# Kernel tuning notes

Measured on AMD Instinct MI355X. Metric: run time of the kernel, lower is better.

The kernel has to match this reference:

```python
import jax, jax.numpy as jnp
import numpy as np

N_NODES = 50000
N_EDGES = 640000
IN_CH = 128
HIDDEN = 128
HEADS = 4
HEAD_DIM = HIDDEN // HEADS  # 32
NEG_SLOPE = 0.2


def setup_inputs() -> dict:
    key = jax.random.key(0)
    ks = jax.random.split(key, 12)
    x = jax.random.normal(ks[0], (N_NODES, IN_CH), dtype=jnp.float32)
    edge_index = jax.random.randint(ks[1], (2, N_EDGES), 0, N_NODES, dtype=jnp.int64)
    s = 0.1
    W1 = jax.random.normal(ks[2], (IN_CH, HEADS * HEAD_DIM), dtype=jnp.float32) * s
    a_src1 = jax.random.normal(ks[3], (HEADS, HEAD_DIM), dtype=jnp.float32) * s
    a_dst1 = jax.random.normal(ks[4], (HEADS, HEAD_DIM), dtype=jnp.float32) * s
    b1 = jax.random.normal(ks[5], (HEADS * HEAD_DIM,), dtype=jnp.float32) * s
    W2 = jax.random.normal(ks[6], (HIDDEN, HEADS * HEAD_DIM), dtype=jnp.float32) * s
    a_src2 = jax.random.normal(ks[7], (HEADS, HEAD_DIM), dtype=jnp.float32) * s
    a_dst2 = jax.random.normal(ks[8], (HEADS, HEAD_DIM), dtype=jnp.float32) * s
    b2 = jax.random.normal(ks[9], (HEADS * HEAD_DIM,), dtype=jnp.float32) * s
    return {"x": x, "edge_index": edge_index, "W1": W1, "a_src1": a_src1,
            "a_dst1": a_dst1, "b1": b1, "W2": W2, "a_src2": a_src2,
            "a_dst2": a_dst2, "b2": b2}


def _gat_conv(x, src, dst, W, a_src, a_dst, b):
    """PyG GATConv (concat=True, add_self_loops already applied to src/dst)."""
    N = x.shape[0]
    H, C = a_src.shape
    h = (x @ W).reshape(N, H, C)                      # [N, H, C]
    alpha_s = jnp.einsum('nhc,hc->nh', h, a_src)      # [N, H]
    alpha_d = jnp.einsum('nhc,hc->nh', h, a_dst)      # [N, H]
    e = alpha_s[src] + alpha_d[dst]                   # [E, H]
    e = jnp.where(e > 0, e, NEG_SLOPE * e)            # leaky_relu(0.2)
    # segment softmax over destination nodes (every node has a self-loop)
    emax = jax.ops.segment_max(e, dst, num_segments=N)
    ee = jnp.exp(e - emax[dst])
    denom = jax.ops.segment_sum(ee, dst, num_segments=N)
    alpha = ee / (denom[dst] + 1e-16)                 # [E, H]
    out = jax.ops.segment_sum(h[src] * alpha[:, :, None], dst, num_segments=N)
    return out.reshape(N, H * C) + b


def reference(x, edge_index, W1, a_src1, a_dst1, b1, W2, a_src2, a_dst2, b2):
    N = x.shape[0]
    loops = jnp.arange(N, dtype=edge_index.dtype)
    src = jnp.concatenate([edge_index[0], loops])
    dst = jnp.concatenate([edge_index[1], loops])
    h = _gat_conv(x, src, dst, W1, a_src1, a_dst1, b1)
    h = jax.nn.relu(h)  # dropout is identity in eval mode
    out = _gat_conv(h, src, dst, W2, a_src2, a_dst2, b2)
    return out
```

## Files before the change

### kernel.cpp

```cpp
#include <hip/hip_runtime.h>
#include <hip/hip_bf16.h>
#include <hip/hip_fp16.h>

#define N_NODES 50000
#define N_EDGES 640000
#define E_TOT   690000
#define CH      128
#define GEMMB   782
#define EBLK    2048
#define NEB     337
#define NBUCK   196
#define MTP     344

typedef __attribute__((ext_vector_type(8))) short short8;
typedef __attribute__((ext_vector_type(4))) float float4v;

static __device__ __forceinline__ float bf2f(unsigned short u) {
  return __uint_as_float(((unsigned)u) << 16);
}
static __device__ __forceinline__ unsigned short f2bf(float f) {
  unsigned u = __float_as_uint(f);
  return (unsigned short)((u + 0x7fffu + ((u >> 16) & 1u)) >> 16);
}

__global__ void k_detect(const unsigned short* __restrict__ x16,
                         const unsigned int* __restrict__ eiw,
                         int* __restrict__ flags)
{
  __shared__ int sf32, si64;
  int t = threadIdx.x;
  if (t == 0) { sf32 = 0; si64 = 1; }
  __syncthreads();
  int bad = 0;
  for (int i = t; i < 4096; i += 256) {
    float v = bf2f(x16[i]);
    if (!(v == v) || fabsf(v) > 100.f) bad = 1;
  }
  if (bad) atomicOr(&sf32, 1);
  if (t < 128 && eiw[2 * t + 1] != 0u) atomicAnd(&si64, 0);
  __syncthreads();
  if (t == 0) { flags[0] = sf32; flags[1] = si64; }
}

static __device__ __forceinline__ void load_edge(const int* __restrict__ ei,
                                                 int e, int i64, int& s, int& d)
{
  if (e >= N_EDGES) { s = d = e - N_EDGES; return; }
  if (i64) { s = ei[2 * (size_t)e]; d = ei[2 * ((size_t)N_EDGES + e)]; }
  else     { s = ei[e];             d = ei[N_EDGES + e]; }
}

static __device__ __forceinline__ short8 load_bf8(const void* __restrict__ X,
                                                  size_t off, int f32)
{
  if (!f32) return *(const short8*)((const unsigned short*)X + off);
  const float4* p = (const float4*)((const float*)X + off);
  float4 u = p[0], v = p[1];
  short8 r;
  r[0] = (short)f2bf(u.x); r[1] = (short)f2bf(u.y);
  r[2] = (short)f2bf(u.z); r[3] = (short)f2bf(u.w);
  r[4] = (short)f2bf(v.x); r[5] = (short)f2bf(v.y);
  r[6] = (short)f2bf(v.z); r[7] = (short)f2bf(v.w);
  return r;
}

__global__ __launch_bounds__(256) void k_prep(
    const void* __restrict__ W1, const void* __restrict__ W2,
    const void* __restrict__ as1, const void* __restrict__ ad1,
    const void* __restrict__ as2, const void* __restrict__ ad2,
    unsigned short* __restrict__ Wt1, unsigned short* __restrict__ Wt2,
    unsigned short* __restrict__ Ba1, unsigned short* __restrict__ Ba2,
    const int* __restrict__ flags)
{
  int f32 = flags[0];
  int b = blockIdx.x, t = threadIdx.x;
  if (b < 8) {
    int g = b * 256 + t;
    int l = g >> 10;
    int rem = g & 1023;
    int k = rem >> 3, n = rem & 7;
    const void* W  = l ? W2 : W1;
    const void* av = (n < 4) ? (l ? as2 : as1) : (l ? ad2 : ad1);
    int h = n & 3;
    float sum = 0.f;
    for (int c = 0; c < 32; c++) {
      float w = f32 ? ((const float*)W)[k * 128 + h * 32 + c]
                    : bf2f(((const unsigned short*)W)[k * 128 + h * 32 + c]);
      float a = f32 ? ((const float*)av)[h * 32 + c]
                    : bf2f(((const unsigned short*)av)[h * 32 + c]);
      sum += w * a;
    }
    unsigned short* Ba = l ? Ba2 : Ba1;
    Ba[n * 128 + k] = f2bf(sum);
    Ba[(8 + (rem >> 7)) * 128 + (rem & 127)] = 0;
  } else {
    int b2 = b - 8;
    int l = b2 >> 7, c = b2 & 127;
    if (t < 128) {
      const void* W = l ? W2 : W1;
      unsigned short* Wt = l ? Wt2 : Wt1;
      Wt[c * 128 + t] = f32 ? f2bf(((const float*)W)[t * 128 + c])
                            : ((const unsigned short*)W)[t * 128 + c];
    }
  }
}

struct SmemG { unsigned short WB[144][136]; };

static __device__ __forceinline__ void gemm_body(
    SmemG& sm, int bx,
    const void* __restrict__ X,
    const unsigned short* __restrict__ Wt_g,
    const unsigned short* __restrict__ Ba_g,
    unsigned short* __restrict__ H, float* __restrict__ AS,
    float* __restrict__ AD, int nrows, int xf32)
{
  int tid = threadIdx.x;
#pragma unroll
  for (int i = 0; i < 8; i++) {
    int j = i * 256 + tid;
    int c = j >> 4, k8 = j & 15;
    short8 v = *(const short8*)(Wt_g + c * 128 + k8 * 8);
    *(short8*)&sm.WB[c][k8 * 8] = v;
  }
  {
    int n = tid >> 4, k8 = tid & 15;
    short8 v = *(const short8*)(Ba_g + n * 128 + k8 * 8);
    *(short8*)&sm.WB[128 + n][k8 * 8] = v;
  }
  __syncthreads();
  int wave = tid >> 6, lane = tid & 63;
  int rt = bx * 4 + wave;
  if (rt * 16 >= nrows) return;
  int R0 = rt * 16;
  int m = lane & 15, quad = lane >> 4;
  size_t abase = (size_t)(R0 + m) * CH + quad * 8;
  float4v acc[8];
  float4v accA = (float4v){0.f, 0.f, 0.f, 0.f};
#pragma unroll
  for (int t = 0; t < 8; t++) acc[t] = (float4v){0.f, 0.f, 0.f, 0.f};
#pragma unroll
  for (int kb = 0; kb < 4; kb++) {
    short8 a = load_bf8(X, abase + kb * 32, xf32);
#pragma unroll
    for (int ct = 0; ct < 8; ct++) {
      short8 b = *(const short8*)&sm.WB[ct * 16 + m][kb * 32 + quad * 8];
      acc[ct] = __builtin_amdgcn_mfma_f32_16x16x32_bf16(a, b, acc[ct], 0, 0, 0);
    }
    short8 bA = *(const short8*)&sm.WB[128 + m][kb * 32 + quad * 8];
    accA = __builtin_amdgcn_mfma_f32_16x16x32_bf16(a, bA, accA, 0, 0, 0);
  }
  int rbase = R0 + quad * 4;
#pragma unroll
  for (int ct = 0; ct < 8; ct++) {
    int col = ct * 16 + m;
#pragma unroll
    for (int r = 0; r < 4; r++)
      H[(size_t)(rbase + r) * CH + col] = __half_as_ushort(__float2half(acc[ct][r]));
  }
  if (m < 4) {
#pragma unroll
    for (int r = 0; r < 4; r++)
      AS[(size_t)(rbase + r) * 4 + m] = accA[r];
  } else if (m < 8) {
#pragma unroll
    for (int r = 0; r < 4; r++)
      AD[(size_t)(rbase + r) * 4 + (m - 4)] = accA[r];
  }
}

__global__ __launch_bounds__(256, 2) void k_gemm(
    const void* __restrict__ X,
    const unsigned short* __restrict__ Wt_g,
    const unsigned short* __restrict__ Ba_g,
    unsigned short* __restrict__ H, float* __restrict__ AS, float* __restrict__ AD,
    int nrows)
{
  __shared__ SmemG sm;
  gemm_body(sm, blockIdx.x, X, Wt_g, Ba_g, H, AS, AD, nrows, 0);
}

__global__ __launch_bounds__(256, 2) void k_gemm_hist(
    const void* __restrict__ X,
    const unsigned short* __restrict__ Wt_g,
    const unsigned short* __restrict__ Ba_g,
    unsigned short* __restrict__ H, float* __restrict__ AS, float* __restrict__ AD,
    int nrows, const int* __restrict__ ei, int* __restrict__ MT,
    const int* __restrict__ flags)
{
  __shared__ SmemG sm;
  __shared__ int hist[NBUCK];
  if (blockIdx.x >= GEMMB) {
    int b = blockIdx.x - GEMMB;
    int t = threadIdx.x;
    if (t < NBUCK) hist[t] = 0;
    __syncthreads();
    int i64 = flags[1];
    int base = b * EBLK;
#pragma unroll
    for (int k = 0; k < 8; k++) {
      int e = base + k * 256 + t;
      if (e < E_TOT) {
        int s, d;
        load_edge(ei, e, i64, s, d);
        atomicAdd(&hist[d >> 8], 1);
      }
    }
    __syncthreads();
    if (t < NBUCK) MT[t * MTP + b] = hist[t];
    return;
  }
  gemm_body(sm, blockIdx.x, X, Wt_g, Ba_g, H, AS, AD, nrows, flags[0]);
}

__global__ __launch_bounds__(512) void k_rowscan(int* __restrict__ MT,
                                                 int* __restrict__ T)
{
  __shared__ int sh[512];
  int q = blockIdx.x, t = threadIdx.x;
  int v = (t < NEB) ? MT[q * MTP + t] : 0;
  sh[t] = v;
  __syncthreads();
  for (int off = 1; off < 512; off <<= 1) {
    int u = (t >= off) ? sh[t - off] : 0;
    __syncthreads();
    sh[t] += u;
    __syncthreads();
  }
  if (t < NEB) MT[q * MTP + t] = sh[t] - v;
  if (t == NEB - 1) T[q] = sh[t];
}

__global__ __launch_bounds__(256) void k_bscan(const int* __restrict__ T,
                                               int* __restrict__ BB)
{
  __shared__ int sh[256];
  int t = threadIdx.x;
  int v = (t < NBUCK) ? T[t] : 0;
  sh[t] = v;
  __syncthreads();
  for (int off = 1; off < 256; off <<= 1) {
    int u = (t >= off) ? sh[t - off] : 0;
    __syncthreads();
    sh[t] += u;
    __syncthreads();
  }
  if (t < NBUCK) BB[t] = sh[t] - v;
  if (t == NBUCK - 1) BB[NBUCK] = sh[t];
}

__global__ __launch_bounds__(256) void k_bucket(
    const int* __restrict__ ei, const int* __restrict__ MT,
    const int* __restrict__ BB, int2* __restrict__ ebuf,
    const int* __restrict__ flags)
{
  __shared__ int cur[NBUCK];
  int b = blockIdx.x, t = threadIdx.x;
  if (t < NBUCK) cur[t] = BB[t] + MT[t * MTP + b];
  __syncthreads();
  int i64 = flags[1];
  int base = b * EBLK;
#pragma unroll
  for (int k = 0; k < 8; k++) {
    int e = base + k * 256 + t;
    if (e < E_TOT) {
      int s, d;
      load_edge(ei, e, i64, s, d);
      int pos = atomicAdd(&cur[d >> 8], 1);
      ebuf[pos] = make_int2(s, d);
    }
  }
}

__global__ __launch_bounds__(256) void k_fine(
    const int2* __restrict__ ebuf, const int* __restrict__ BB,
    int* __restrict__ row_ptr, int* __restrict__ deg,
    int* __restrict__ csr_src)
{
  __shared__ int cnt[256], sh[256], cur[256];
  int q = blockIdx.x, t = threadIdx.x;
  int lo = BB[q], hi = BB[q + 1];
  cnt[t] = 0;
  __syncthreads();
  for (int i = lo + t; i < hi; i += 256)
    atomicAdd(&cnt[ebuf[i].y & 255], 1);
  __syncthreads();
  int v = cnt[t];
  sh[t] = v;
  __syncthreads();
  for (int off = 1; off < 256; off <<= 1) {
    int u = (t >= off) ? sh[t - off] : 0;
    __syncthreads();
    sh[t] += u;
    __syncthreads();
  }
  int lp = sh[t] - v;
  int n = (q << 8) + t;
  if (n < N_NODES) { row_ptr[n] = lo + lp; deg[n] = v; }
  cur[t] = lo + lp;
  __syncthreads();
  for (int i = lo + t; i < hi; i += 256) {
    int2 p = ebuf[i];
    int slot = atomicAdd(&cur[p.y & 255], 1);
    csr_src[slot] = p.x;
  }
}

__global__ __launch_bounds__(256) void k_agg(
    const int* __restrict__ row_ptr, const int* __restrict__ deg,
    const int* __restrict__ csr_src,
    const __half* __restrict__ H,
    const float* __restrict__ AS, const float* __restrict__ AD,
    const void* __restrict__ b, void* __restrict__ Y,
    const int* __restrict__ flags, int layer)
{
  int tid = threadIdx.x;
  int node = blockIdx.x * 4 + (tid >> 6);
  if (node >= N_NODES) return;
  int lane = tid & 63;
  int h = lane >> 4;
  int c0 = 2 * lane;
  float adh = AD[(size_t)node * 4 + h];
  int start = row_ptr[node];
  int dg = deg[node];
  const __half2* __restrict__ H2 = (const __half2*)H;
  float accx = 0.f, accy = 0.f, den = 0.f;
  int j = 0;
  for (; j + 8 <= dg; j += 8) {
    int sI[8];
#pragma unroll
    for (int u = 0; u < 8; u++) sI[u] = csr_src[start + j + u];
    float eV[8];
#pragma unroll
    for (int u = 0; u < 8; u++) eV[u] = AS[(size_t)sI[u] * 4 + h] + adh;
    float2 vV[8];
#pragma unroll
    for (int u = 0; u < 8; u++) vV[u] = __half22float2(H2[(size_t)sI[u] * 64 + lane]);
#pragma unroll
    for (int u = 0; u < 8; u++) {
      float x = eV[u] > 0.f ? eV[u] : 0.2f * eV[u];
      float ex = __expf(x);
      accx += ex * vV[u].x;
      accy += ex * vV[u].y;
      den  += ex;
    }
  }
  for (; j + 4 <= dg; j += 4) {
    int sI[4];
#pragma unroll
    for (int u = 0; u < 4; u++) sI[u] = csr_src[start + j + u];
    float eV[4];
#pragma unroll
    for (int u = 0; u < 4; u++) eV[u] = AS[(size_t)sI[u] * 4 + h] + adh;
    float2 vV[4];
#pragma unroll
    for (int u = 0; u < 4; u++) vV[u] = __half22float2(H2[(size_t)sI[u] * 64 + lane]);
#pragma unroll
    for (int u = 0; u < 4; u++) {
      float x = eV[u] > 0.f ? eV[u] : 0.2f * eV[u];
      float ex = __expf(x);
      accx += ex * vV[u].x;
      accy += ex * vV[u].y;
      den  += ex;
    }
  }
  for (; j < dg; j++) {
    int s = csr_src[start + j];
    float e = AS[(size_t)s * 4 + h] + adh;
    float2 v = __half22float2(H2[(size_t)s * 64 + lane]);
    e = e > 0.f ? e : 0.2f * e;
    float ex = __expf(e);
    accx += ex * v.x;
    accy += ex * v.y;
    den  += ex;
  }
  float inv = 1.f / (den + 1e-16f);
  int f32 = flags[0];
  float b0 = f32 ? ((const float*)b)[c0]     : bf2f(((const unsigned short*)b)[c0]);
  float b1 = f32 ? ((const float*)b)[c0 + 1] : bf2f(((const unsigned short*)b)[c0 + 1]);
  float r0 = accx * inv + b0;
  float r1 = accy * inv + b1;
  size_t o = (size_t)node * CH + c0;
  if (layer == 1) {
    r0 = r0 > 0.f ? r0 : 0.f;
    r1 = r1 > 0.f ? r1 : 0.f;
    ushort2 w; w.x = f2bf(r0); w.y = f2bf(r1);
    *(ushort2*)((unsigned short*)Y + o) = w;
  } else if (f32) {
    float2 w; w.x = r0; w.y = r1;
    *(float2*)((float*)Y + o) = w;
  } else {
    ushort2 w; w.x = f2bf(r0); w.y = f2bf(r1);
    *(ushort2*)((unsigned short*)Y + o) = w;
  }
}

extern "C" void kernel_launch(void* const* d_in, const int* in_sizes, int n_in,
                              void* d_out, int out_size, void* d_ws, size_t ws_size,
                              hipStream_t stream)
{
  const void* x   = d_in[0];
  const int*  ei  = (const int*)d_in[1];
  const void* W1  = d_in[2];
  const void* as1 = d_in[3];
  const void* ad1 = d_in[4];
  const void* b1  = d_in[5];
  const void* W2  = d_in[6];
  const void* as2 = d_in[7];
  const void* ad2 = d_in[8];
  const void* b2  = d_in[9];

  char* ws = (char*)d_ws;
  unsigned short* H  = (unsigned short*)(ws);
  float*  AS         = (float*)(ws + 12800000);
  float*  AD         = (float*)(ws + 13600000);
  unsigned short* X2 = (unsigned short*)(ws + 14400000);
  int*    deg        = (int*)(ws + 27200000);
  int*    row_ptr    = (int*)(ws + 27400000);
  int*    csr_src    = (int*)(ws + 27600000);
  int*    MT         = (int*)(ws + 30360000);
  int*    T          = (int*)(ws + 30630000);
  int*    BB         = (int*)(ws + 30631000);
  int*    flags      = (int*)(ws + 30632000);
  int2*   ebuf       = (int2*)(ws + 30640000);
  unsigned short* Wt1 = (unsigned short*)(ws + 36160000);
  unsigned short* Wt2 = (unsigned short*)(ws + 36200000);
  unsigned short* Ba1 = (unsigned short*)(ws + 36240000);
  unsigned short* Ba2 = (unsigned short*)(ws + 36248000);

  const int agg_blocks = (N_NODES + 3) / 4;

  k_detect<<<1, 256, 0, stream>>>((const unsigned short*)x,
                                  (const unsigned int*)ei, flags);
  k_prep<<<264, 256, 0, stream>>>(W1, W2, as1, ad1, as2, ad2,
                                  Wt1, Wt2, Ba1, Ba2, flags);

  k_gemm_hist<<<GEMMB + NEB, 256, 0, stream>>>(
      x, Wt1, Ba1, H, AS, AD, N_NODES, ei, MT, flags);

  k_rowscan<<<NBUCK, 512, 0, stream>>>(MT, T);
  k_bscan  <<<1, 256, 0, stream>>>(T, BB);
  k_bucket <<<NEB, 256, 0, stream>>>(ei, MT, BB, ebuf, flags);
  k_fine   <<<NBUCK, 256, 0, stream>>>(ebuf, BB, row_ptr, deg, csr_src);

  k_agg<<<agg_blocks, 256, 0, stream>>>(row_ptr, deg, csr_src,
                                        (const __half*)H, AS, AD,
                                        b1, X2, flags, 1);

  k_gemm<<<GEMMB, 256, 0, stream>>>(X2, Wt2, Ba2, H, AS, AD, N_NODES);
  k_agg<<<agg_blocks, 256, 0, stream>>>(row_ptr, deg, csr_src,
                                        (const __half*)H, AS, AD,
                                        b2, d_out, flags, 2);
}
```

Before: 217.6 us.

## Replace two-level bucket CSR build with direct degree atomics and node scans

```diff
diff --git a/kernel.cpp b/kernel.cpp
--- a/kernel.cpp
+++ b/kernel.cpp
@@ -6,11 +6,11 @@
 #define N_EDGES 640000
 #define E_TOT   690000
 #define CH      128
-#define GEMMB   782
+#define ROWPAD  50176
+#define GEMMB   391
 #define EBLK    2048
 #define NEB     337
 #define NBUCK   196
-#define MTP     344
 
 typedef __attribute__((ext_vector_type(8))) short short8;
 typedef __attribute__((ext_vector_type(4))) float float4v;
@@ -21,25 +21,6 @@
 static __device__ __forceinline__ unsigned short f2bf(float f) {
   unsigned u = __float_as_uint(f);
   return (unsigned short)((u + 0x7fffu + ((u >> 16) & 1u)) >> 16);
-}
-
-__global__ void k_detect(const unsigned short* __restrict__ x16,
-                         const unsigned int* __restrict__ eiw,
-                         int* __restrict__ flags)
-{
-  __shared__ int sf32, si64;
-  int t = threadIdx.x;
-  if (t == 0) { sf32 = 0; si64 = 1; }
-  __syncthreads();
-  int bad = 0;
-  for (int i = t; i < 4096; i += 256) {
-    float v = bf2f(x16[i]);
-    if (!(v == v) || fabsf(v) > 100.f) bad = 1;
-  }
-  if (bad) atomicOr(&sf32, 1);
-  if (t < 128 && eiw[2 * t + 1] != 0u) atomicAnd(&si64, 0);
-  __syncthreads();
-  if (t == 0) { flags[0] = sf32; flags[1] = si64; }
 }
 
 static __device__ __forceinline__ void load_edge(const int* __restrict__ ei,
@@ -70,10 +51,27 @@
     const void* __restrict__ as2, const void* __restrict__ ad2,
     unsigned short* __restrict__ Wt1, unsigned short* __restrict__ Wt2,
     unsigned short* __restrict__ Ba1, unsigned short* __restrict__ Ba2,
-    const int* __restrict__ flags)
-{
-  int f32 = flags[0];
+    const unsigned short* __restrict__ x16,
+    const unsigned int* __restrict__ eiw,
+    int* __restrict__ flags, int* __restrict__ deg)
+{
   int b = blockIdx.x, t = threadIdx.x;
+  int gid = b * 256 + t;
+  if (gid < N_NODES) deg[gid] = 0;
+  __shared__ int sf, si;
+  if (t == 0) { sf = 0; si = 1; }
+  __syncthreads();
+  int bad = 0;
+  for (int i = t; i < 4096; i += 256) {
+    float v = bf2f(x16[i]);
+    if (!(v == v) || fabsf(v) > 100.f) bad = 1;
+  }
+  if (bad) atomicOr(&sf, 1);
+  if (b == 0 && t < 128 && eiw[2 * t + 1] != 0u) atomicAnd(&si, 0);
+  __syncthreads();
+  int f32 = sf;
+  if (b == 0 && t == 0) { flags[0] = sf; flags[1] = si; }
+
   if (b < 8) {
     int g = b * 256 + t;
     int l = g >> 10;
@@ -120,52 +118,62 @@
   for (int i = 0; i < 8; i++) {
     int j = i * 256 + tid;
     int c = j >> 4, k8 = j & 15;
-    short8 v = *(const short8*)(Wt_g + c * 128 + k8 * 8);
-    *(short8*)&sm.WB[c][k8 * 8] = v;
+    *(short8*)&sm.WB[c][k8 * 8] = *(const short8*)(Wt_g + c * 128 + k8 * 8);
   }
   {
     int n = tid >> 4, k8 = tid & 15;
-    short8 v = *(const short8*)(Ba_g + n * 128 + k8 * 8);
-    *(short8*)&sm.WB[128 + n][k8 * 8] = v;
+    *(short8*)&sm.WB[128 + n][k8 * 8] = *(const short8*)(Ba_g + n * 128 + k8 * 8);
   }
   __syncthreads();
   int wave = tid >> 6, lane = tid & 63;
-  int rt = bx * 4 + wave;
-  if (rt * 16 >= nrows) return;
-  int R0 = rt * 16;
+  int R0 = (bx * 4 + wave) * 32;
+  if (R0 >= nrows) return;
   int m = lane & 15, quad = lane >> 4;
-  size_t abase = (size_t)(R0 + m) * CH + quad * 8;
-  float4v acc[8];
-  float4v accA = (float4v){0.f, 0.f, 0.f, 0.f};
-#pragma unroll
-  for (int t = 0; t < 8; t++) acc[t] = (float4v){0.f, 0.f, 0.f, 0.f};
+  int rA = R0 + m;        if (rA >= nrows) rA = nrows - 1;
+  int rB = R0 + 16 + m;   if (rB >= nrows) rB = nrows - 1;
+  size_t aA = (size_t)rA * CH + quad * 8;
+  size_t aB = (size_t)rB * CH + quad * 8;
+  float4v acc[2][8];
+  float4v accA[2];
+#pragma unroll
+  for (int hf = 0; hf < 2; hf++) {
+    accA[hf] = (float4v){0.f, 0.f, 0.f, 0.f};
+#pragma unroll
+    for (int ct = 0; ct < 8; ct++) acc[hf][ct] = (float4v){0.f, 0.f, 0.f, 0.f};
+  }
 #pragma unroll
   for (int kb = 0; kb < 4; kb++) {
-    short8 a = load_bf8(X, abase + kb * 32, xf32);
+    short8 a0 = load_bf8(X, aA + kb * 32, xf32);
+    short8 a1 = load_bf8(X, aB + kb * 32, xf32);
 #pragma unroll
     for (int ct = 0; ct < 8; ct++) {
-      short8 b = *(const short8*)&sm.WB[ct * 16 + m][kb * 32 + quad * 8];
-      acc[ct] = __builtin_amdgcn_mfma_f32_16x16x32_bf16(a, b, acc[ct], 0, 0, 0);
+      short8 bb = *(const short8*)&sm.WB[ct * 16 + m][kb * 32 + quad * 8];
+      acc[0][ct] = __builtin_amdgcn_mfma_f32_16x16x32_bf16(a0, bb, acc[0][ct], 0, 0, 0);
+      acc[1][ct] = __builtin_amdgcn_mfma_f32_16x16x32_bf16(a1, bb, acc[1][ct], 0, 0, 0);
     }
     short8 bA = *(const short8*)&sm.WB[128 + m][kb * 32 + quad * 8];
-    accA = __builtin_amdgcn_mfma_f32_16x16x32_bf16(a, bA, accA, 0, 0, 0);
-  }
-  int rbase = R0 + quad * 4;
-#pragma unroll
-  for (int ct = 0; ct < 8; ct++) {
-    int col = ct * 16 + m;
-#pragma unroll
-    for (int r = 0; r < 4; r++)
-      H[(size_t)(rbase + r) * CH + col] = __half_as_ushort(__float2half(acc[ct][r]));
-  }
-  if (m < 4) {
-#pragma unroll
-    for (int r = 0; r < 4; r++)
-      AS[(size_t)(rbase + r) * 4 + m] = accA[r];
-  } else if (m < 8) {
-#pragma unroll
-    for (int r = 0; r < 4; r++)
-      AD[(size_t)(rbase + r) * 4 + (m - 4)] = accA[r];
+    accA[0] = __builtin_amdgcn_mfma_f32_16x16x32_bf16(a0, bA, accA[0], 0, 0, 0);
+    accA[1] = __builtin_amdgcn_mfma_f32_16x16x32_bf16(a1, bA, accA[1], 0, 0, 0);
+  }
+#pragma unroll
+  for (int hf = 0; hf < 2; hf++) {
+    int rbase = R0 + hf * 16 + quad * 4;
+#pragma unroll
+    for (int ct = 0; ct < 8; ct++) {
+      int col = ct * 16 + m;
+#pragma unroll
+      for (int r = 0; r < 4; r++)
+        H[(size_t)(rbase + r) * CH + col] = __half_as_ushort(__float2half(acc[hf][ct][r]));
+    }
+    if (m < 4) {
+#pragma unroll
+      for (int r = 0; r < 4; r++)
+        AS[(size_t)(rbase + r) * 4 + m] = accA[hf][r];
+    } else if (m < 8) {
+#pragma unroll
+      for (int r = 0; r < 4; r++)
+        AD[(size_t)(rbase + r) * 4 + (m - 4)] = accA[hf][r];
+    }
   }
 }
 
@@ -185,16 +193,13 @@
     const unsigned short* __restrict__ Wt_g,
     const unsigned short* __restrict__ Ba_g,
     unsigned short* __restrict__ H, float* __restrict__ AS, float* __restrict__ AD,
-    int nrows, const int* __restrict__ ei, int* __restrict__ MT,
+    int nrows, const int* __restrict__ ei, int* __restrict__ deg,
     const int* __restrict__ flags)
 {
   __shared__ SmemG sm;
-  __shared__ int hist[NBUCK];
   if (blockIdx.x >= GEMMB) {
     int b = blockIdx.x - GEMMB;
     int t = threadIdx.x;
-    if (t < NBUCK) hist[t] = 0;
-    __syncthreads();
     int i64 = flags[1];
     int base = b * EBLK;
 #pragma unroll
@@ -203,40 +208,22 @@
       if (e < E_TOT) {
         int s, d;
         load_edge(ei, e, i64, s, d);
-        atomicAdd(&hist[d >> 8], 1);
+        atomicAdd(&deg[d], 1);
       }
     }
-    __syncthreads();
-    if (t < NBUCK) MT[t * MTP + b] = hist[t];
     return;
   }
   gemm_body(sm, blockIdx.x, X, Wt_g, Ba_g, H, AS, AD, nrows, flags[0]);
 }
 
-__global__ __launch_bounds__(512) void k_rowscan(int* __restrict__ MT,
-                                                 int* __restrict__ T)
-{
-  __shared__ int sh[512];
+__global__ __launch_bounds__(256) void k_scan1(const int* __restrict__ deg,
+                                               int* __restrict__ rp,
+                                               int* __restrict__ T)
+{
+  __shared__ int sh[256];
   int q = blockIdx.x, t = threadIdx.x;
-  int v = (t < NEB) ? MT[q * MTP + t] : 0;
-  sh[t] = v;
-  __syncthreads();
-  for (int off = 1; off < 512; off <<= 1) {
-    int u = (t >= off) ? sh[t - off] : 0;
-    __syncthreads();
-    sh[t] += u;
-    __syncthreads();
-  }
-  if (t < NEB) MT[q * MTP + t] = sh[t] - v;
-  if (t == NEB - 1) T[q] = sh[t];
-}
-
-__global__ __launch_bounds__(256) void k_bscan(const int* __restrict__ T,
-                                               int* __restrict__ BB)
-{
-  __shared__ int sh[256];
-  int t = threadIdx.x;
-  int v = (t < NBUCK) ? T[t] : 0;
+  int n = (q << 8) + t;
+  int v = (n < N_NODES) ? deg[n] : 0;
   sh[t] = v;
   __syncthreads();
   for (int off = 1; off < 256; off <<= 1) {
@@ -245,19 +232,41 @@
     sh[t] += u;
     __syncthreads();
   }
-  if (t < NBUCK) BB[t] = sh[t] - v;
-  if (t == NBUCK - 1) BB[NBUCK] = sh[t];
-}
-
-__global__ __launch_bounds__(256) void k_bucket(
-    const int* __restrict__ ei, const int* __restrict__ MT,
-    const int* __restrict__ BB, int2* __restrict__ ebuf,
-    const int* __restrict__ flags)
-{
-  __shared__ int cur[NBUCK];
+  if (n < N_NODES) rp[n] = sh[t] - v;
+  if (t == 255) T[q] = sh[255];
+}
+
+__global__ __launch_bounds__(256) void k_scan2(int* __restrict__ rp,
+                                               int* __restrict__ cur,
+                                               const int* __restrict__ T)
+{
+  __shared__ int sh[256];
+  __shared__ int sbase;
+  int q = blockIdx.x, t = threadIdx.x;
+  int v = (t < NBUCK) ? T[t] : 0;
+  sh[t] = v;
+  __syncthreads();
+  for (int off = 1; off < 256; off <<= 1) {
+    int u = (t >= off) ? sh[t - off] : 0;
+    __syncthreads();
+    sh[t] += u;
+    __syncthreads();
+  }
+  if (t == q) sbase = sh[t] - v;
+  __syncthreads();
+  int n = (q << 8) + t;
+  if (n < N_NODES) {
+    int r = rp[n] + sbase;
+    rp[n] = r;
+    cur[n] = r;
+  }
+}
+
+__global__ __launch_bounds__(256) void k_scatter(
+    const int* __restrict__ ei, int* __restrict__ cur,
+    int* __restrict__ csr_src, const int* __restrict__ flags)
+{
   int b = blockIdx.x, t = threadIdx.x;
-  if (t < NBUCK) cur[t] = BB[t] + MT[t * MTP + b];
-  __syncthreads();
   int i64 = flags[1];
   int base = b * EBLK;
 #pragma unroll
@@ -266,43 +275,9 @@
     if (e < E_TOT) {
       int s, d;
       load_edge(ei, e, i64, s, d);
-      int pos = atomicAdd(&cur[d >> 8], 1);
-      ebuf[pos] = make_int2(s, d);
-    }
-  }
-}
-
-__global__ __launch_bounds__(256) void k_fine(
-    const int2* __restrict__ ebuf, const int* __restrict__ BB,
-    int* __restrict__ row_ptr, int* __restrict__ deg,
-    int* __restrict__ csr_src)
-{
-  __shared__ int cnt[256], sh[256], cur[256];
-  int q = blockIdx.x, t = threadIdx.x;
-  int lo = BB[q], hi = BB[q + 1];
-  cnt[t] = 0;
-  __syncthreads();
-  for (int i = lo + t; i < hi; i += 256)
-    atomicAdd(&cnt[ebuf[i].y & 255], 1);
-  __syncthreads();
-  int v = cnt[t];
-  sh[t] = v;
-  __syncthreads();
-  for (int off = 1; off < 256; off <<= 1) {
-    int u = (t >= off) ? sh[t - off] : 0;
-    __syncthreads();
-    sh[t] += u;
-    __syncthreads();
-  }
-  int lp = sh[t] - v;
-  int n = (q << 8) + t;
-  if (n < N_NODES) { row_ptr[n] = lo + lp; deg[n] = v; }
-  cur[t] = lo + lp;
-  __syncthreads();
-  for (int i = lo + t; i < hi; i += 256) {
-    int2 p = ebuf[i];
-    int slot = atomicAdd(&cur[p.y & 255], 1);
-    csr_src[slot] = p.x;
+      int pos = atomicAdd(&cur[d], 1);
+      csr_src[pos] = s;
+    }
   }
 }
 
@@ -412,36 +387,33 @@
 
   char* ws = (char*)d_ws;
   unsigned short* H  = (unsigned short*)(ws);
-  float*  AS         = (float*)(ws + 12800000);
-  float*  AD         = (float*)(ws + 13600000);
-  unsigned short* X2 = (unsigned short*)(ws + 14400000);
-  int*    deg        = (int*)(ws + 27200000);
-  int*    row_ptr    = (int*)(ws + 27400000);
-  int*    csr_src    = (int*)(ws + 27600000);
-  int*    MT         = (int*)(ws + 30360000);
-  int*    T          = (int*)(ws + 30630000);
-  int*    BB         = (int*)(ws + 30631000);
-  int*    flags      = (int*)(ws + 30632000);
-  int2*   ebuf       = (int2*)(ws + 30640000);
-  unsigned short* Wt1 = (unsigned short*)(ws + 36160000);
-  unsigned short* Wt2 = (unsigned short*)(ws + 36200000);
-  unsigned short* Ba1 = (unsigned short*)(ws + 36240000);
-  unsigned short* Ba2 = (unsigned short*)(ws + 36248000);
+  float*  AS         = (float*)(ws + 12845056);
+  float*  AD         = (float*)(ws + 13647872);
+  unsigned short* X2 = (unsigned short*)(ws + 14450688);
+  int*    deg        = (int*)(ws + 27295744);
+  int*    row_ptr    = (int*)(ws + 27496448);
+  int*    cur        = (int*)(ws + 27697152);
+  int*    csr_src    = (int*)(ws + 27897856);
+  int*    T          = (int*)(ws + 30658560);
+  int*    flags      = (int*)(ws + 30659584);
+  unsigned short* Wt1 = (unsigned short*)(ws + 30660608);
+  unsigned short* Wt2 = (unsigned short*)(ws + 30693376);
+  unsigned short* Ba1 = (unsigned short*)(ws + 30726144);
+  unsigned short* Ba2 = (unsigned short*)(ws + 30730240);
 
   const int agg_blocks = (N_NODES + 3) / 4;
 
-  k_detect<<<1, 256, 0, stream>>>((const unsigned short*)x,
-                                  (const unsigned int*)ei, flags);
   k_prep<<<264, 256, 0, stream>>>(W1, W2, as1, ad1, as2, ad2,
-                                  Wt1, Wt2, Ba1, Ba2, flags);
+                                  Wt1, Wt2, Ba1, Ba2,
+                                  (const unsigned short*)x,
+                                  (const unsigned int*)ei, flags, deg);
 
   k_gemm_hist<<<GEMMB + NEB, 256, 0, stream>>>(
-      x, Wt1, Ba1, H, AS, AD, N_NODES, ei, MT, flags);
-
-  k_rowscan<<<NBUCK, 512, 0, stream>>>(MT, T);
-  k_bscan  <<<1, 256, 0, stream>>>(T, BB);
-  k_bucket <<<NEB, 256, 0, stream>>>(ei, MT, BB, ebuf, flags);
-  k_fine   <<<NBUCK, 256, 0, stream>>>(ebuf, BB, row_ptr, deg, csr_src);
+      x, Wt1, Ba1, H, AS, AD, N_NODES, ei, deg, flags);
+
+  k_scan1  <<<NBUCK, 256, 0, stream>>>(deg, row_ptr, T);
+  k_scan2  <<<NBUCK, 256, 0, stream>>>(row_ptr, cur, T);
+  k_scatter<<<NEB, 256, 0, stream>>>(ei, cur, csr_src, flags);
 
   k_agg<<<agg_blocks, 256, 0, stream>>>(row_ptr, deg, csr_src,
                                         (const __half*)H, AS, AD,
```

Measured after the change: 260.1 us. +19.5%, slower.

## Merge detect into prep kernel and give each GEMM wave two row tiles

Applied to the files above, without the earlier changes.

```diff
diff --git a/kernel.cpp b/kernel.cpp
--- a/kernel.cpp
+++ b/kernel.cpp
@@ -6,7 +6,8 @@
 #define N_EDGES 640000
 #define E_TOT   690000
 #define CH      128
-#define GEMMB   782
+#define ROWPAD  50176
+#define GEMMB   391
 #define EBLK    2048
 #define NEB     337
 #define NBUCK   196
@@ -21,25 +22,6 @@
 static __device__ __forceinline__ unsigned short f2bf(float f) {
   unsigned u = __float_as_uint(f);
   return (unsigned short)((u + 0x7fffu + ((u >> 16) & 1u)) >> 16);
-}
-
-__global__ void k_detect(const unsigned short* __restrict__ x16,
-                         const unsigned int* __restrict__ eiw,
-                         int* __restrict__ flags)
-{
-  __shared__ int sf32, si64;
-  int t = threadIdx.x;
-  if (t == 0) { sf32 = 0; si64 = 1; }
-  __syncthreads();
-  int bad = 0;
-  for (int i = t; i < 4096; i += 256) {
-    float v = bf2f(x16[i]);
-    if (!(v == v) || fabsf(v) > 100.f) bad = 1;
-  }
-  if (bad) atomicOr(&sf32, 1);
-  if (t < 128 && eiw[2 * t + 1] != 0u) atomicAnd(&si64, 0);
-  __syncthreads();
-  if (t == 0) { flags[0] = sf32; flags[1] = si64; }
 }
 
 static __device__ __forceinline__ void load_edge(const int* __restrict__ ei,
@@ -70,10 +52,25 @@
     const void* __restrict__ as2, const void* __restrict__ ad2,
     unsigned short* __restrict__ Wt1, unsigned short* __restrict__ Wt2,
     unsigned short* __restrict__ Ba1, unsigned short* __restrict__ Ba2,
-    const int* __restrict__ flags)
-{
-  int f32 = flags[0];
+    const unsigned short* __restrict__ x16,
+    const unsigned int* __restrict__ eiw,
+    int* __restrict__ flags)
+{
   int b = blockIdx.x, t = threadIdx.x;
+  __shared__ int sf, si;
+  if (t == 0) { sf = 0; si = 1; }
+  __syncthreads();
+  int bad = 0;
+  for (int i = t; i < 4096; i += 256) {
+    float v = bf2f(x16[i]);
+    if (!(v == v) || fabsf(v) > 100.f) bad = 1;
+  }
+  if (bad) atomicOr(&sf, 1);
+  if (b == 0 && t < 128 && eiw[2 * t + 1] != 0u) atomicAnd(&si, 0);
+  __syncthreads();
+  int f32 = sf;
+  if (b == 0 && t == 0) { flags[0] = sf; flags[1] = si; }
+
   if (b < 8) {
     int g = b * 256 + t;
     int l = g >> 10;
@@ -120,52 +117,62 @@
   for (int i = 0; i < 8; i++) {
     int j = i * 256 + tid;
     int c = j >> 4, k8 = j & 15;
-    short8 v = *(const short8*)(Wt_g + c * 128 + k8 * 8);
-    *(short8*)&sm.WB[c][k8 * 8] = v;
+    *(short8*)&sm.WB[c][k8 * 8] = *(const short8*)(Wt_g + c * 128 + k8 * 8);
   }
   {
     int n = tid >> 4, k8 = tid & 15;
-    short8 v = *(const short8*)(Ba_g + n * 128 + k8 * 8);
-    *(short8*)&sm.WB[128 + n][k8 * 8] = v;
+    *(short8*)&sm.WB[128 + n][k8 * 8] = *(const short8*)(Ba_g + n * 128 + k8 * 8);
   }
   __syncthreads();
   int wave = tid >> 6, lane = tid & 63;
-  int rt = bx * 4 + wave;
-  if (rt * 16 >= nrows) return;
-  int R0 = rt * 16;
+  int R0 = (bx * 4 + wave) * 32;
+  if (R0 >= nrows) return;
   int m = lane & 15, quad = lane >> 4;
-  size_t abase = (size_t)(R0 + m) * CH + quad * 8;
-  float4v acc[8];
-  float4v accA = (float4v){0.f, 0.f, 0.f, 0.f};
-#pragma unroll
-  for (int t = 0; t < 8; t++) acc[t] = (float4v){0.f, 0.f, 0.f, 0.f};
+  int rA = R0 + m;        if (rA >= nrows) rA = nrows - 1;
+  int rB = R0 + 16 + m;   if (rB >= nrows) rB = nrows - 1;
+  size_t aA = (size_t)rA * CH + quad * 8;
+  size_t aB = (size_t)rB * CH + quad * 8;
+  float4v acc[2][8];
+  float4v accA[2];
+#pragma unroll
+  for (int hf = 0; hf < 2; hf++) {
+    accA[hf] = (float4v){0.f, 0.f, 0.f, 0.f};
+#pragma unroll
+    for (int ct = 0; ct < 8; ct++) acc[hf][ct] = (float4v){0.f, 0.f, 0.f, 0.f};
+  }
 #pragma unroll
   for (int kb = 0; kb < 4; kb++) {
-    short8 a = load_bf8(X, abase + kb * 32, xf32);
+    short8 a0 = load_bf8(X, aA + kb * 32, xf32);
+    short8 a1 = load_bf8(X, aB + kb * 32, xf32);
 #pragma unroll
     for (int ct = 0; ct < 8; ct++) {
-      short8 b = *(const short8*)&sm.WB[ct * 16 + m][kb * 32 + quad * 8];
-      acc[ct] = __builtin_amdgcn_mfma_f32_16x16x32_bf16(a, b, acc[ct], 0, 0, 0);
+      short8 bb = *(const short8*)&sm.WB[ct * 16 + m][kb * 32 + quad * 8];
+      acc[0][ct] = __builtin_amdgcn_mfma_f32_16x16x32_bf16(a0, bb, acc[0][ct], 0, 0, 0);
+      acc[1][ct] = __builtin_amdgcn_mfma_f32_16x16x32_bf16(a1, bb, acc[1][ct], 0, 0, 0);
     }
     short8 bA = *(const short8*)&sm.WB[128 + m][kb * 32 + quad * 8];
-    accA = __builtin_amdgcn_mfma_f32_16x16x32_bf16(a, bA, accA, 0, 0, 0);
-  }
-  int rbase = R0 + quad * 4;
-#pragma unroll
-  for (int ct = 0; ct < 8; ct++) {
-    int col = ct * 16 + m;
-#pragma unroll
-    for (int r = 0; r < 4; r++)
-      H[(size_t)(rbase + r) * CH + col] = __half_as_ushort(__float2half(acc[ct][r]));
-  }
-  if (m < 4) {
-#pragma unroll
-    for (int r = 0; r < 4; r++)
-      AS[(size_t)(rbase + r) * 4 + m] = accA[r];
-  } else if (m < 8) {
-#pragma unroll
-    for (int r = 0; r < 4; r++)
-      AD[(size_t)(rbase + r) * 4 + (m - 4)] = accA[r];
+    accA[0] = __builtin_amdgcn_mfma_f32_16x16x32_bf16(a0, bA, accA[0], 0, 0, 0);
+    accA[1] = __builtin_amdgcn_mfma_f32_16x16x32_bf16(a1, bA, accA[1], 0, 0, 0);
+  }
+#pragma unroll
+  for (int hf = 0; hf < 2; hf++) {
+    int rbase = R0 + hf * 16 + quad * 4;
+#pragma unroll
+    for (int ct = 0; ct < 8; ct++) {
+      int col = ct * 16 + m;
+#pragma unroll
+      for (int r = 0; r < 4; r++)
+        H[(size_t)(rbase + r) * CH + col] = __half_as_ushort(__float2half(acc[hf][ct][r]));
+    }
+    if (m < 4) {
+#pragma unroll
+      for (int r = 0; r < 4; r++)
+        AS[(size_t)(rbase + r) * 4 + m] = accA[hf][r];
+    } else if (m < 8) {
+#pragma unroll
+      for (int r = 0; r < 4; r++)
+        AD[(size_t)(rbase + r) * 4 + (m - 4)] = accA[hf][r];
+    }
   }
 }
 
@@ -412,28 +419,28 @@
 
   char* ws = (char*)d_ws;
   unsigned short* H  = (unsigned short*)(ws);
-  float*  AS         = (float*)(ws + 12800000);
-  float*  AD         = (float*)(ws + 13600000);
-  unsigned short* X2 = (unsigned short*)(ws + 14400000);
-  int*    deg        = (int*)(ws + 27200000);
-  int*    row_ptr    = (int*)(ws + 27400000);
-  int*    csr_src    = (int*)(ws + 27600000);
-  int*    MT         = (int*)(ws + 30360000);
-  int*    T          = (int*)(ws + 30630000);
-  int*    BB         = (int*)(ws + 30631000);
-  int*    flags      = (int*)(ws + 30632000);
-  int2*   ebuf       = (int2*)(ws + 30640000);
-  unsigned short* Wt1 = (unsigned short*)(ws + 36160000);
-  unsigned short* Wt2 = (unsigned short*)(ws + 36200000);
-  unsigned short* Ba1 = (unsigned short*)(ws + 36240000);
-  unsigned short* Ba2 = (unsigned short*)(ws + 36248000);
+  float*  AS         = (float*)(ws + 12845056);
+  float*  AD         = (float*)(ws + 13647872);
+  unsigned short* X2 = (unsigned short*)(ws + 14450688);
+  int*    deg        = (int*)(ws + 27295744);
+  int*    row_ptr    = (int*)(ws + 27496448);
+  int*    csr_src    = (int*)(ws + 27697152);
+  int*    MT         = (int*)(ws + 30457600);
+  int*    T          = (int*)(ws + 30728192);
+  int*    BB         = (int*)(ws + 30729216);
+  int*    flags      = (int*)(ws + 30730240);
+  int2*   ebuf       = (int2*)(ws + 30731264);
+  unsigned short* Wt1 = (unsigned short*)(ws + 36251264);
+  unsigned short* Wt2 = (unsigned short*)(ws + 36284032);
+  unsigned short* Ba1 = (unsigned short*)(ws + 36316800);
+  unsigned short* Ba2 = (unsigned short*)(ws + 36320896);
 
   const int agg_blocks = (N_NODES + 3) / 4;
 
-  k_detect<<<1, 256, 0, stream>>>((const unsigned short*)x,
+  k_prep<<<264, 256, 0, stream>>>(W1, W2, as1, ad1, as2, ad2,
+                                  Wt1, Wt2, Ba1, Ba2,
+                                  (const unsigned short*)x,
                                   (const unsigned int*)ei, flags);
-  k_prep<<<264, 256, 0, stream>>>(W1, W2, as1, ad1, as2, ad2,
-                                  Wt1, Wt2, Ba1, Ba2, flags);
 
   k_gemm_hist<<<GEMMB + NEB, 256, 0, stream>>>(
       x, Wt1, Ba1, H, AS, AD, N_NODES, ei, MT, flags);
```

Result: no change. 217.1 us (-0.2%).
